# Kernel tuning notes

Measured on AMD Instinct MI355X. Metric: run time of the kernel, lower is better.

## Reference

```python
import jax, jax.numpy as jnp
import numpy as np

K = 3
KK = K * K


def conv3x3(x, w, b):
    # x: [B,C,H,W], w: [O,C,3,3]
    y = jax.lax.conv_general_dilated(x, w, (1, 1), ((1, 1), (1, 1)),
                                     dimension_numbers=('NCHW', 'OIHW', 'NCHW'))
    return y + b[None, :, None, None]


def deform_conv(x, offset, w, b):
    # torchvision.ops.deform_conv2d, 3x3, pad=1, stride=1, no mask.
    B, C, H, W = x.shape
    off = offset.reshape(B, KK, 2, H, W)  # per kernel tap: (dy, dx)
    ky = jnp.repeat(jnp.arange(K, dtype=x.dtype) - 1, K)  # [9]
    kx = jnp.tile(jnp.arange(K, dtype=x.dtype) - 1, K)
    py = jnp.arange(H, dtype=x.dtype)[None, None, :, None] + ky[None, :, None, None] + off[:, :, 0]
    px = jnp.arange(W, dtype=x.dtype)[None, None, None, :] + kx[None, :, None, None] + off[:, :, 1]
    y0 = jnp.floor(py)
    x0 = jnp.floor(px)
    wy = (py - y0)[:, None]  # [B,1,9,H,W]
    wx = (px - x0)[:, None]
    y0i = y0.astype(jnp.int32)
    x0i = x0.astype(jnp.int32)
    xf = x.reshape(B, C, H * W)

    def corner(yi, xi):
        valid = ((yi >= 0) & (yi < H) & (xi >= 0) & (xi < W))
        idx = jnp.clip(yi, 0, H - 1) * W + jnp.clip(xi, 0, W - 1)  # [B,9,H,W]
        g = jax.vmap(lambda xb, ib: xb[:, ib.reshape(-1)])(xf, idx)  # [B,C,9*H*W]
        return g.reshape(B, C, KK, H, W) * valid[:, None].astype(x.dtype)

    val = (corner(y0i, x0i) * (1 - wy) * (1 - wx)
           + corner(y0i, x0i + 1) * (1 - wy) * wx
           + corner(y0i + 1, x0i) * wy * (1 - wx)
           + corner(y0i + 1, x0i + 1) * wy * wx)  # [B,C,9,H,W]
    out = jnp.einsum('bckhw,ock->bohw', val, w.reshape(w.shape[0], C, KK))
    return out + b[None, :, None, None]


def se_gate(x, w1, b1, w2, b2):
    # global avg pool -> 1x1 conv -> relu -> 1x1 conv -> sigmoid -> scale
    m = x.mean((2, 3))  # [B,C]
    h = jax.nn.relu(jnp.einsum('bc,rc->br', m, w1) + b1)
    g = jax.nn.sigmoid(jnp.einsum('br,cr->bc', h, w2) + b2)
    return x * g[:, :, None, None]


def resize_bilinear(x, oh, ow):
    # F.interpolate(mode='bilinear', align_corners=False)
    B, C, H, W = x.shape

    def coords(n_in, n_out):
        src = (jnp.arange(n_out, dtype=x.dtype) + 0.5) * (n_in / n_out) - 0.5
        src = jnp.clip(src, 0.0, n_in - 1)
        i0 = jnp.floor(src).astype(jnp.int32)
        i1 = jnp.minimum(i0 + 1, n_in - 1)
        return i0, i1, (src - i0).astype(x.dtype)

    y0, y1, wy = coords(H, oh)
    x = x[:, :, y0, :] * (1 - wy)[None, None, :, None] + x[:, :, y1, :] * wy[None, None, :, None]
    c0, c1, wc = coords(W, ow)
    x = x[:, :, :, c0] * (1 - wc)[None, None, None, :] + x[:, :, :, c1] * wc[None, None, None, :]
    return x


def setup_inputs() -> dict:
    key = jax.random.key(0)
    ks = jax.random.split(key, 12)
    B, C, H, W = 4, 64, 128, 128
    L, O, R = 4, 64, 4  # levels, out_channels, reduction=64//16
    d = {
        'x': jax.random.normal(ks[0], (B, C, H, W), jnp.float32),
        'off_w': jax.random.normal(ks[1], (L, 2 * KK, C, 3, 3), jnp.float32) * 0.01,
        'off_b': jax.random.normal(ks[2], (L, 2 * KK), jnp.float32) * 0.01,
        'dc_w': jax.random.normal(ks[3], (L, O, C, 3, 3), jnp.float32) * 0.05,
        'dc_b': jax.random.normal(ks[4], (L, O), jnp.float32) * 0.05,
        'se_w1': jax.random.normal(ks[5], (L, R, O), jnp.float32) * 0.1,
        'se_b1': jax.random.normal(ks[6], (L, R), jnp.float32) * 0.1,
        'se_w2': jax.random.normal(ks[7], (L, O, R), jnp.float32) * 0.1,
        'se_b2': jax.random.normal(ks[8], (L, O), jnp.float32) * 0.1,
        'fuse_w': jax.random.normal(ks[9], (O, L * O), jnp.float32) * 0.05,
        'fuse_b': jax.random.normal(ks[10], (O,), jnp.float32) * 0.05,
    }
    return d


def reference(x, off_w, off_b, dc_w, dc_b, se_w1, se_b1, se_w2, se_b2, fuse_w, fuse_b):
    B, _, H, W = x.shape
    L = off_w.shape[0]
    cur = x
    feats = []
    for i in range(L):
        if i > 0:
            cur = resize_bilinear(cur, cur.shape[2] // 2, cur.shape[3] // 2)
        off = conv3x3(cur, off_w[i], off_b[i])
        cur = deform_conv(cur, off, dc_w[i], dc_b[i])
        cur = se_gate(cur, se_w1[i], se_b1[i], se_w2[i], se_b2[i])
        feats.append(resize_bilinear(cur, H, W))
    for i in range(L - 2, -1, -1):
        feats[i] = feats[i] + feats[i + 1]
    fused = jnp.concatenate(feats, axis=1)  # [B, L*O, H, W]
    return jnp.einsum('bchw,oc->bohw', fused, fuse_w) + fuse_b[None, :, None, None]
```

## Files before the change

### kernel.cpp

```cpp
#include <hip/hip_runtime.h>
#include <hip/hip_bf16.h>
#include <math.h>


constexpr int Bn = 4;

typedef __attribute__((ext_vector_type(8))) short short8;
typedef __attribute__((ext_vector_type(4))) float f32x4;
typedef __attribute__((ext_vector_type(4))) unsigned uint4v;
typedef __attribute__((ext_vector_type(4))) unsigned short ushort4v;

static __device__ __forceinline__ short f2b(float f){
  union { float f; unsigned u; } v; v.f = f;
  unsigned r = v.u + 0x7fffu + ((v.u >> 16) & 1u);
  return (short)(r >> 16);
}
static __device__ __forceinline__ unsigned f2b2(float x, float y){
  union { __hip_bfloat162 h; unsigned u; } cv;
  cv.h = __float22bfloat162_rn(make_float2(x, y));
  return cv.u;
}
static __device__ __forceinline__ float blo(unsigned u){ return __uint_as_float(u << 16); }
static __device__ __forceinline__ float bhi(unsigned u){ return __uint_as_float(u & 0xffff0000u); }

constexpr size_t OFF_CUR   = 0;
constexpr size_t OFF_DC    = OFF_CUR  + 4194304;
constexpr size_t OFF_T0    = OFF_DC   + 4194304;
constexpr size_t OFF_T1    = OFF_T0   + 4194304;
constexpr size_t OFF_T2    = OFF_T1   + 1048576;
constexpr size_t OFF_T3    = OFF_T2   + 262144;
constexpr size_t OFF_WSUMT = OFF_T3   + 65536;
constexpr size_t OFF_DCWT  = OFF_WSUMT + 8192;
constexpr size_t OFF_OWT   = OFF_DCWT  + 73728;
constexpr size_t OFF_SUMS  = OFF_OWT   + 36864;

__global__ __launch_bounds__(256) void prepcvt_k(
    const float* __restrict__ dc_w, const float* __restrict__ off_w,
    const float* __restrict__ fuse_w, float* __restrict__ ws,
    const float* __restrict__ x, unsigned* __restrict__ cur){
  __shared__ float t[64][65];
  {
    int i = blockIdx.x * 256 + threadIdx.x;
    short* dcwT  = (short*)(ws + OFF_DCWT);
    short* owT   = (short*)(ws + OFF_OWT);
    short* wsumT = (short*)(ws + OFF_WSUMT);
    if (i < 147456){
      int oc = i / 576, r = i % 576, k = r >> 6, c = r & 63;
      dcwT[i] = f2b(dc_w[(oc*64 + c)*9 + k]);
    } else if (i < 147456 + 73728){
      int tt = i - 147456;
      int lm = tt / 576, l = lm >> 5, m = lm & 31, r = tt % 576, k = r >> 6, c = r & 63;
      owT[tt] = (m < 18) ? f2b(off_w[((l*18 + m)*64 + c)*9 + k]) : (short)0;
    } else if (i < 147456 + 73728 + 16384){
      int tt = i - (147456 + 73728);
      int l = tt / 4096, r = tt % 4096, o = r / 64, c = r % 64;
      float s = 0.f;
      for (int jl = 0; jl <= l; jl++) s += fuse_w[o*256 + jl*64 + c];
      wsumT[tt] = f2b(s);
    } else if (i < 147456 + 73728 + 16384 + 65536){
      ws[OFF_SUMS + (i - (147456 + 73728 + 16384))] = 0.f;
    }
  }
  if (blockIdx.x < 1024){
    int tile = blockIdx.x;
    int b = tile >> 8, p0 = (tile & 255) << 6;
    int tx = threadIdx.x & 63, ty = threadIdx.x >> 6;
    #pragma unroll
    for (int c = ty; c < 64; c += 4)
      t[c][tx] = x[(((size_t)(b << 6) + c) << 14) + p0 + tx];
    __syncthreads();
    int u = threadIdx.x & 31, pr = threadIdx.x >> 5;
    #pragma unroll
    for (int i = 0; i < 8; i++){
      int pp = pr + i*8;
      unsigned v = f2b2(t[2*u][pp], t[2*u + 1][pp]);
      cur[((size_t)(b << 14) + p0 + pp)*32 + u] = v;
    }
  }
}

template<int H, int LVL>
__global__ __launch_bounds__(256, 3) void deform8_k(
    const unsigned* __restrict__ cur, const float* __restrict__ ws_all,
    const float* __restrict__ off_bias, const float* __restrict__ dc_bias,
    float* __restrict__ dc, float* __restrict__ sums){
  constexpr int W = H, P = H * W;
  constexpr int PITCHB = 584 * 2;
  constexpr int TPR8 = W/8, TPB8 = P/64;
  __shared__ __align__(16) short valA[16][584];
  __shared__ __align__(16) char  patchS[64*144];
  __shared__ __align__(16) float4 tapW[144];
  __shared__ __align__(8)  unsigned short tapIs[144][4];
  float* offsP = (float*)((char*)&valA[0][0] + 8192);
  const short* owt = (const short*)(ws_all + OFF_OWT) + LVL * 32 * 576;
  const short* dcw = (const short*)(ws_all + OFF_DCWT) + (size_t)LVL * 64 * 576;
  const int tid = threadIdx.x;
  const int wave = tid >> 6, lane = tid & 63;
  const int c0 = lane & 15, quad = lane >> 4, q4 = quad * 4;
  const int b = blockIdx.x / TPB8;
  const int rr = blockIdx.x % TPB8;
  const int hrow8 = (rr / TPR8) * 8, wcol8 = (rr % TPR8) * 8;
  const unsigned* curu = cur + (size_t)b * P * 32;
  const int n = wave*16 + c0;
  const float bt2 = dc_bias[LVL*64 + n];
  const int tk = tid % 9, tp = tid / 9;
  float oby = 0.f, obx = 0.f;
  if (tid < 144){
    oby = off_bias[LVL*18 + 2*tk];
    obx = off_bias[LVL*18 + 2*tk + 1];
  }
  const int pl = lane >> 3, cq = lane & 7;

  #pragma unroll 1
  for (int t = 0; t < 4; t++){
    const int srow = hrow8 + (t >> 1)*4, scol = wcol8 + (t & 1)*4;
    if (t) __syncthreads();

    #pragma unroll
    for (int i = 0; i < 2; i++){
      int pp = wave*16 + i*8 + pl;
      int R = pp >> 3, C = pp & 7;
      int yy = srow - 2 + R, xx = scol - 2 + C;
      bool v = ((unsigned)yy < (unsigned)H) & ((unsigned)xx < (unsigned)W);
      int idx = v ? (yy*W + xx) : 0;
      uint4 d = *(const uint4*)((const char*)curu + (size_t)idx*128 + cq*16);
      if (!v){ d.x = 0; d.y = 0; d.z = 0; d.w = 0; }
      *(uint4*)(patchS + pp*144 + cq*16) = d;
    }
    __syncthreads();

    {
      const int colw = wave & 1, kh = wave >> 1;
      const char* pb = patchS + (((c0 >> 2) + 1)*8 + (c0 & 3) + 1)*144 + quad*16;
      const short* wrow = owt + (colw*16 + c0)*576 + quad*8;
      f32x4 oacc = {0,0,0,0};
      if (kh == 0){
        #pragma unroll
        for (int kb = 0; kb < 9; kb++){
          const int tap = kb >> 1;
          short8 a  = *(const short8*)(pb + ((tap/3)*8 + (tap%3))*144 + (kb&1)*64);
          short8 bf = *(const short8*)&wrow[kb*32];
          oacc = __builtin_amdgcn_mfma_f32_16x16x32_bf16(a, bf, oacc, 0, 0, 0);
        }
      } else {
        #pragma unroll
        for (int kb = 0; kb < 9; kb++){
          const int kk = 9 + kb, tap = kk >> 1;
          short8 a  = *(const short8*)(pb + ((tap/3)*8 + (tap%3))*144 + (kk&1)*64);
          short8 bf = *(const short8*)&wrow[kk*32];
          oacc = __builtin_amdgcn_mfma_f32_16x16x32_bf16(a, bf, oacc, 0, 0, 0);
        }
      }
      int comp = colw*16 + c0;
      if (comp < 18){
        #pragma unroll
        for (int r = 0; r < 4; r++) offsP[kh*288 + (q4 + r)*18 + comp] = oacc[r];
      }
    }
    __syncthreads();

    if (tid < 144){
      int p = tp, k = tk;
      int h = srow + (p >> 2), w = scol + (p & 3);
      float oy = offsP[p*18 + 2*k]     + offsP[288 + p*18 + 2*k]     + oby;
      float ox = offsP[p*18 + 2*k + 1] + offsP[288 + p*18 + 2*k + 1] + obx;
      float py = (float)(h + k/3 - 1) + oy;
      float px = (float)(w + k%3 - 1) + ox;
      float y0f = floorf(py), x0f = floorf(px);
      float fy = py - y0f, fx = px - x0f;
      int y0 = (int)y0f, x0 = (int)x0f, y1 = y0 + 1, x1 = x0 + 1;
      bool vy0 = (y0 >= 0) & (y0 < H), vy1 = (y1 >= 0) & (y1 < H);
      bool vx0 = (x0 >= 0) & (x0 < W), vx1 = (x1 >= 0) & (x1 < W);
      int y0c = min(max(y0, 0), H-1), y1c = min(max(y1, 0), H-1);
      int x0c = min(max(x0, 0), W-1), x1c = min(max(x1, 0), W-1);
      float gy = 1.f - fy, gx = 1.f - fx;
      tapW[tid] = make_float4((vy0 & vx0) ? gy*gx : 0.f,
                              (vy0 & vx1) ? gy*fx : 0.f,
                              (vy1 & vx0) ? fy*gx : 0.f,
                              (vy1 & vx1) ? fy*fx : 0.f);
      int ry = y0 - srow + 2, rx = x0 - scol + 2;
      if (((unsigned)ry < 7u) & ((unsigned)rx < 7u)){
        tapIs[tid][0] = (unsigned short)(0x8000u | (ry*8 + rx));
      } else {
        tapIs[tid][0] = (unsigned short)(y0c*W + x0c);
        tapIs[tid][1] = (unsigned short)(y0c*W + x1c);
        tapIs[tid][2] = (unsigned short)(y1c*W + x0c);
        tapIs[tid][3] = (unsigned short)(y1c*W + x1c);
      }
    }
    __syncthreads();

    {
      const char* curc8 = (const char*)curu + c0*8;
      int T = wave*36 + quad;
      int p = wave*4, k = quad;
      #pragma unroll
      for (int i = 0; i < 9; i++){
        float4 wv = tapW[T];
        unsigned short t0 = tapIs[T][0];
        uint2 u0, u1, u2, u3;
        if (t0 & 0x8000u){
          const char* pb2 = patchS + (int)(t0 & 0x7fffu)*144 + c0*8;
          u0 = *(const uint2*)(pb2);
          u1 = *(const uint2*)(pb2 + 144);
          u2 = *(const uint2*)(pb2 + 144*8);
          u3 = *(const uint2*)(pb2 + 144*9);
        } else {
          uint2 tw = *(const uint2*)tapIs[T];
          u0 = *(const uint2*)(curc8 + ((size_t)(tw.x & 0xffffu) << 7));
          u1 = *(const uint2*)(curc8 + ((size_t)(tw.x >> 16)     << 7));
          u2 = *(const uint2*)(curc8 + ((size_t)(tw.y & 0xffffu) << 7));
          u3 = *(const uint2*)(curc8 + ((size_t)(tw.y >> 16)     << 7));
        }
        float a0 = wv.x*blo(u0.x) + wv.y*blo(u1.x) + wv.z*blo(u2.x) + wv.w*blo(u3.x);
        float a1 = wv.x*bhi(u0.x) + wv.y*bhi(u1.x) + wv.z*bhi(u2.x) + wv.w*bhi(u3.x);
        float a2 = wv.x*blo(u0.y) + wv.y*blo(u1.y) + wv.z*blo(u2.y) + wv.w*blo(u3.y);
        float a3 = wv.x*bhi(u0.y) + wv.y*bhi(u1.y) + wv.z*bhi(u2.y) + wv.w*bhi(u3.y);
        uint2 pk; pk.x = f2b2(a0, a1); pk.y = f2b2(a2, a3);
        *(uint2*)((char*)&valA[0][0] + p*PITCHB + k*128 + c0*8) = pk;
        T += 4; k += 4; if (k >= 9){ k -= 9; ++p; }
      }
    }
    __syncthreads();

    f32x4 d0 = {bt2, bt2, bt2, bt2}, d1 = {0,0,0,0};
    #pragma unroll
    for (int kb = 0; kb < 9; kb++){
      short8 a  = *(const short8*)&valA[c0][kb*32 + quad*8];
      short8 bf = *(const short8*)&dcw[n*576 + kb*32 + quad*8];
      d0 = __builtin_amdgcn_mfma_f32_16x16x32_bf16(a, bf, d0, 0, 0, 0);
    }
    #pragma unroll
    for (int kb = 9; kb < 18; kb++){
      short8 a  = *(const short8*)&valA[c0][kb*32 + quad*8];
      short8 bf = *(const short8*)&dcw[n*576 + kb*32 + quad*8];
      d1 = __builtin_amdgcn_mfma_f32_16x16x32_bf16(a, bf, d1, 0, 0, 0);
    }
    f32x4 acc;
    #pragma unroll
    for (int r = 0; r < 4; r++) acc[r] = d0[r] + d1[r];
    float* dcb = dc + ((size_t)b*P + (size_t)(srow + quad)*W + scol)*64;
    #pragma unroll
    for (int r = 0; r < 4; r++) dcb[r*64 + n] = acc[r];
    float s = acc[0] + acc[1] + acc[2] + acc[3];
    s += __shfl_xor(s, 16);
    s += __shfl_xor(s, 32);
    if (quad == 0) atomicAdd(&sums[(LVL*16 + (blockIdx.x & 15))*256 + (b << 6) + n], s);
  }
}

template<int H, int LVL>
__global__ __launch_bounds__(256, 7) void deform_k(
    const unsigned* __restrict__ cur, const float* __restrict__ ws_all,
    const float* __restrict__ off_bias, const float* __restrict__ dc_bias,
    float* __restrict__ dc, float* __restrict__ sums){
  constexpr int W = H, P = H * W;
  constexpr int PITCHB = 584 * 2;
  constexpr int TPR = W/4, TPB = P/16;
  __shared__ __align__(16) short valA[16][584];
  __shared__ __align__(16) float4 tapW[144];
  __shared__ __align__(8)  unsigned short tapIs[144][4];
  short* patch = &valA[0][0];
  float* offsP = (float*)((char*)&valA[0][0] + 8192);
  const short* owt = (const short*)(ws_all + OFF_OWT) + LVL * 32 * 576;
  const short* dcw = (const short*)(ws_all + OFF_DCWT) + (size_t)LVL * 64 * 576;
  const int tid = threadIdx.x;
  const int wave = tid >> 6, lane = tid & 63;
  const int c0 = lane & 15, quad = lane >> 4, q4 = quad * 4;
  const int b = blockIdx.x / TPB;
  const int rr = blockIdx.x % TPB;
  const int hrow = (rr / TPR) * 4, wcol = (rr % TPR) * 4;
  const unsigned* curu = cur + (size_t)b * P * 32;

  {
    #pragma unroll
    for (int i = 0; i < 3; i++){
      if (i < 2 || quad == 0){
        int p36 = wave*9 + i*4 + quad;
        int r6 = p36 / 6, c6 = p36 - r6*6;
        int yy = hrow - 1 + r6, xx = wcol - 1 + c6;
        bool v = ((unsigned)yy < (unsigned)H) & ((unsigned)xx < (unsigned)W);
        int idx = v ? (yy*W + xx) : 0;
        uint2 d = *(const uint2*)(curu + (size_t)idx*32 + c0*2);
        if (!v){ d.x = 0u; d.y = 0u; }
        *(uint2*)(patch + p36*72 + c0*4) = d;
      }
    }
  }
  __syncthreads();

  {
    const int colw = wave & 1, kh = wave >> 1;
    const char* pb = (const char*)patch + ((c0 >> 2) * 6 + (c0 & 3)) * 144 + quad * 16;
    const short* wrow = owt + (colw*16 + c0)*576 + quad*8;
    f32x4 oacc = {0,0,0,0};
    if (kh == 0){
      #pragma unroll
      for (int kb = 0; kb < 9; kb++){
        const int tap = kb >> 1;
        short8 a  = *(const short8*)(pb + ((tap/3)*864 + (tap%3)*144 + (kb&1)*64));
        short8 bf = *(const short8*)&wrow[kb*32];
        oacc = __builtin_amdgcn_mfma_f32_16x16x32_bf16(a, bf, oacc, 0, 0, 0);
      }
    } else {
      #pragma unroll
      for (int kb = 0; kb < 9; kb++){
        const int kk = 9 + kb, tap = kk >> 1;
        short8 a  = *(const short8*)(pb + ((tap/3)*864 + (tap%3)*144 + (kk&1)*64));
        short8 bf = *(const short8*)&wrow[kk*32];
        oacc = __builtin_amdgcn_mfma_f32_16x16x32_bf16(a, bf, oacc, 0, 0, 0);
      }
    }
    int comp = colw*16 + c0;
    if (comp < 18){
      #pragma unroll
      for (int r = 0; r < 4; r++) offsP[kh*288 + (q4 + r)*18 + comp] = oacc[r];
    }
  }
  __syncthreads();

  if (tid < 144){
    int p = tid / 9, k = tid % 9;
    int h = hrow + (p >> 2), w = wcol + (p & 3);
    float oy = offsP[p*18 + 2*k]     + offsP[288 + p*18 + 2*k]     + off_bias[LVL*18 + 2*k];
    float ox = offsP[p*18 + 2*k + 1] + offsP[288 + p*18 + 2*k + 1] + off_bias[LVL*18 + 2*k + 1];
    float py = (float)(h + k/3 - 1) + oy;
    float px = (float)(w + k%3 - 1) + ox;
    float y0f = floorf(py), x0f = floorf(px);
    float fy = py - y0f, fx = px - x0f;
    int y0 = (int)y0f, x0 = (int)x0f, y1 = y0 + 1, x1 = x0 + 1;
    bool vy0 = (y0 >= 0) & (y0 < H), vy1 = (y1 >= 0) & (y1 < H);
    bool vx0 = (x0 >= 0) & (x0 < W), vx1 = (x1 >= 0) & (x1 < W);
    int y0c = min(max(y0, 0), H-1), y1c = min(max(y1, 0), H-1);
    int x0c = min(max(x0, 0), W-1), x1c = min(max(x1, 0), W-1);
    float gy = 1.f - fy, gx = 1.f - fx;
    tapW[tid] = make_float4((vy0 & vx0) ? gy*gx : 0.f,
                            (vy0 & vx1) ? gy*fx : 0.f,
                            (vy1 & vx0) ? fy*gx : 0.f,
                            (vy1 & vx1) ? fy*fx : 0.f);
    ushort4v ti = { (unsigned short)(y0c*W + x0c), (unsigned short)(y0c*W + x1c),
                    (unsigned short)(y1c*W + x0c), (unsigned short)(y1c*W + x1c) };
    *(ushort4v*)tapIs[tid] = ti;
  }
  __syncthreads();

  {
    const char* curc8 = (const char*)curu + c0*8;
    int T = wave*36 + quad;
    int p = T/9, k = T - p*9;
    #pragma unroll
    for (int i = 0; i < 9; i++){
      float4 wv = tapW[T];
      uint2 tw = *(const uint2*)tapIs[T];
      uint2 u0 = *(const uint2*)(curc8 + ((size_t)(tw.x & 0xffffu) << 7));
      uint2 u1 = *(const uint2*)(curc8 + ((size_t)(tw.x >> 16) << 7));
      uint2 u2 = *(const uint2*)(curc8 + ((size_t)(tw.y & 0xffffu) << 7));
      uint2 u3 = *(const uint2*)(curc8 + ((size_t)(tw.y >> 16) << 7));
      float a0 = wv.x*blo(u0.x) + wv.y*blo(u1.x) + wv.z*blo(u2.x) + wv.w*blo(u3.x);
      float a1 = wv.x*bhi(u0.x) + wv.y*bhi(u1.x) + wv.z*bhi(u2.x) + wv.w*bhi(u3.x);
      float a2 = wv.x*blo(u0.y) + wv.y*blo(u1.y) + wv.z*blo(u2.y) + wv.w*blo(u3.y);
      float a3 = wv.x*bhi(u0.y) + wv.y*bhi(u1.y) + wv.z*bhi(u2.y) + wv.w*bhi(u3.y);
      uint2 pk; pk.x = f2b2(a0, a1); pk.y = f2b2(a2, a3);
      *(uint2*)((char*)&valA[0][0] + p*PITCHB + k*128 + c0*8) = pk;
      T += 4; k += 4; if (k >= 9){ k -= 9; ++p; }
    }
  }
  __syncthreads();

  const int n = wave*16 + c0;
  float bt2 = dc_bias[LVL*64 + n];
  f32x4 d0 = {bt2, bt2, bt2, bt2}, d1 = {0,0,0,0};
  #pragma unroll
  for (int kb = 0; kb < 9; kb++){
    short8 a  = *(const short8*)&valA[c0][kb*32 + quad*8];
    short8 bf = *(const short8*)&dcw[n*576 + kb*32 + quad*8];
    d0 = __builtin_amdgcn_mfma_f32_16x16x32_bf16(a, bf, d0, 0, 0, 0);
  }
  #pragma unroll
  for (int kb = 9; kb < 18; kb++){
    short8 a  = *(const short8*)&valA[c0][kb*32 + quad*8];
    short8 bf = *(const short8*)&dcw[n*576 + kb*32 + quad*8];
    d1 = __builtin_amdgcn_mfma_f32_16x16x32_bf16(a, bf, d1, 0, 0, 0);
  }
  f32x4 acc;
  #pragma unroll
  for (int r = 0; r < 4; r++) acc[r] = d0[r] + d1[r];
  float* dcb = dc + ((size_t)b*P + (size_t)(hrow + quad)*W + wcol)*64;
  #pragma unroll
  for (int r = 0; r < 4; r++) dcb[r*64 + n] = acc[r];
  float s = acc[0] + acc[1] + acc[2] + acc[3];
  s += __shfl_xor(s, 16);
  s += __shfl_xor(s, 32);
  if (quad == 0) atomicAdd(&sums[(LVL*16 + (blockIdx.x & 15))*256 + (b << 6) + n], s);
}

template<int W, int LVL>
__global__ __launch_bounds__(256) void fuse_gd_k(
    const float* __restrict__ dcv, const float* __restrict__ sums,
    const float* __restrict__ se_w1, const float* __restrict__ se_b1,
    const float* __restrict__ se_w2, const float* __restrict__ se_b2,
    const float* __restrict__ ws_all, float* __restrict__ tmp, unsigned* __restrict__ curn){
  constexpr int P = W * W;
  constexpr bool POOL = (LVL < 3);
  constexpr float invP = 1.f / (float)P;
  __shared__ __align__(16) float fS[64][68];
  __shared__ __align__(16) float gsh[64];
  const short* wsl = (const short*)(ws_all + OFF_WSUMT) + LVL * 4096;
  const int tid = threadIdx.x, wave = tid >> 6, lane = tid & 63;
  const int c0 = lane & 15, quad = lane >> 4, q4 = quad * 4;
  int b, rp = 0, cs = 0;
  if (POOL){
    constexpr int tilesPerB = P / 64, tilesPerRow = W / 32;
    b = blockIdx.x / tilesPerB;
    int r = blockIdx.x % tilesPerB;
    rp = r / tilesPerRow; cs = r % tilesPerRow;
  } else {
    b = (blockIdx.x * 64) / P;
  }

  {
    int sg = tid >> 6, c = tid & 63;
    float part = 0.f;
    #pragma unroll
    for (int s = 0; s < 4; s++) part += sums[(LVL*16 + sg*4 + s)*256 + (b << 6) + c];
    fS[sg][c] = part;
    __syncthreads();
    if (tid < 64){
      int r = tid & 3, j = tid >> 2;
      float hp = 0.f;
      #pragma unroll
      for (int q = 0; q < 4; q++){
        int cq = j*4 + q;
        float m = (fS[0][cq] + fS[1][cq] + fS[2][cq] + fS[3][cq]) * invP;
        hp += m * se_w1[(LVL*4 + r)*64 + cq];
      }
      hp += __shfl_xor(hp, 4);  hp += __shfl_xor(hp, 8);
      hp += __shfl_xor(hp, 16); hp += __shfl_xor(hp, 32);
      float hr = fmaxf(hp + se_b1[LVL*4 + r], 0.f);
      float a = se_b2[LVL*64 + tid];
      #pragma unroll
      for (int r2 = 0; r2 < 4; r2++)
        a += __shfl(hr, r2) * se_w2[(LVL*64 + tid)*4 + r2];
      gsh[tid] = 1.f / (1.f + expf(-a));
    }
    __syncthreads();
  }

  float4 g4 = *(const float4*)&gsh[c0*4];
  #pragma unroll
  for (int i = 0; i < 4; i++){
    int lp = wave*16 + (lane >> 4) + i*4;
    size_t gpix = POOL ? ((size_t)b*P + (size_t)(2*rp + (lp >> 5))*W + cs*32 + (lp & 31))
                       : ((size_t)blockIdx.x*64 + lp);
    float4 d = *(const float4*)&dcv[gpix*64 + c0*4];
    float4 v = make_float4(d.x*g4.x, d.y*g4.y, d.z*g4.z, d.w*g4.w);
    *(float4*)&fS[lp][c0*4] = v;
  }
  __syncthreads();
  f32x4 acc[4] = {{0,0,0,0},{0,0,0,0},{0,0,0,0},{0,0,0,0}};
  #pragma unroll
  for (int kb = 0; kb < 2; kb++){
    float4 lo = *(const float4*)&fS[wave*16 + c0][kb*32 + quad*8];
    float4 hi = *(const float4*)&fS[wave*16 + c0][kb*32 + quad*8 + 4];
    uint4v ua = {f2b2(lo.x, lo.y), f2b2(lo.z, lo.w), f2b2(hi.x, hi.y), f2b2(hi.z, hi.w)};
    short8 a = __builtin_bit_cast(short8, ua);
    #pragma unroll
    for (int t = 0; t < 4; t++){
      short8 bf = *(const short8*)&wsl[(t*16 + c0)*64 + kb*32 + quad*8];
      acc[t] = __builtin_amdgcn_mfma_f32_16x16x32_bf16(a, bf, acc[t], 0, 0, 0);
    }
  }
  #pragma unroll
  for (int t = 0; t < 4; t++){
    int n = t*16 + c0;
    size_t plane = ((size_t)(b << 6) + n) * P;
    size_t pix = POOL ? ((size_t)(2*rp + (wave >> 1))*W + cs*32 + (wave & 1)*16 + q4)
                      : ((size_t)(blockIdx.x*64) - (size_t)b*P + wave*16 + q4);
    *(f32x4*)&tmp[plane + pix] = acc[t];
  }
  if constexpr (POOL){
    int j = tid >> 4, uu = tid & 15;
    float4 p0 = *(const float4*)&fS[2*j][uu*4];
    float4 p1 = *(const float4*)&fS[2*j + 1][uu*4];
    float4 p2 = *(const float4*)&fS[32 + 2*j][uu*4];
    float4 p3 = *(const float4*)&fS[33 + 2*j][uu*4];
    float4 av = make_float4(0.25f*(p0.x + p1.x + p2.x + p3.x),
                            0.25f*(p0.y + p1.y + p2.y + p3.y),
                            0.25f*(p0.z + p1.z + p2.z + p3.z),
                            0.25f*(p0.w + p1.w + p2.w + p3.w));
    uint2 pv = make_uint2(f2b2(av.x, av.y), f2b2(av.z, av.w));
    *(uint2*)&curn[((size_t)b*(P/4) + (size_t)rp*(W/2) + cs*16 + j)*32 + uu*2] = pv;
  }
}

__global__ void final_k(const float* __restrict__ ws_all, const float* __restrict__ fuse_bias,
                        float* __restrict__ out){
  int i = blockIdx.x * 256 + threadIdx.x;
  int w = i & 127, h = (i >> 7) & 127, o = (i >> 14) & 63, b = i >> 20;
  float acc = fuse_bias[o] + ws_all[OFF_T0 + (((size_t)(b << 6) + o) << 14) + (h << 7) + w];
  const float* tarr[3] = {ws_all + OFF_T1, ws_all + OFF_T2, ws_all + OFF_T3};
  #pragma unroll
  for (int li = 0; li < 3; li++){
    int l = li + 1, Hl = 128 >> l;
    float scale = 1.0f / (float)(1 << l);
    float sy = fminf(fmaxf((h + 0.5f)*scale - 0.5f, 0.f), (float)(Hl - 1));
    float sx = fminf(fmaxf((w + 0.5f)*scale - 0.5f, 0.f), (float)(Hl - 1));
    int y0 = (int)sy, x0 = (int)sx;
    float fy = sy - y0, fx = sx - x0;
    int y1 = min(y0 + 1, Hl - 1), x1 = min(x0 + 1, Hl - 1);
    const float* tb = tarr[li] + (size_t)((b << 6) + o) * Hl * Hl;
    float v00 = tb[y0*Hl + x0], v01 = tb[y0*Hl + x1];
    float v10 = tb[y1*Hl + x0], v11 = tb[y1*Hl + x1];
    acc += (1.f-fy)*((1.f-fx)*v00 + fx*v01) + fy*((1.f-fx)*v10 + fx*v11);
  }
  out[i] = acc;
}

extern "C" void kernel_launch(void* const* d_in, const int* in_sizes, int n_in,
                              void* d_out, int out_size, void* d_ws, size_t ws_size,
                              hipStream_t stream){
  (void)in_sizes; (void)n_in; (void)out_size; (void)ws_size;
  const float* x      = (const float*)d_in[0];
  const float* off_w  = (const float*)d_in[1];
  const float* off_b  = (const float*)d_in[2];
  const float* dc_w   = (const float*)d_in[3];
  const float* dc_b   = (const float*)d_in[4];
  const float* se_w1  = (const float*)d_in[5];
  const float* se_b1  = (const float*)d_in[6];
  const float* se_w2  = (const float*)d_in[7];
  const float* se_b2  = (const float*)d_in[8];
  const float* fuse_w = (const float*)d_in[9];
  const float* fuse_b = (const float*)d_in[10];
  float* out = (float*)d_out;
  float* ws = (float*)d_ws;
  unsigned* cur = (unsigned*)(ws + OFF_CUR);
  float* dc   = ws + OFF_DC;
  float* tmp[4] = {ws + OFF_T0, ws + OFF_T1, ws + OFF_T2, ws + OFF_T3};
  float* sums = ws + OFF_SUMS;

  prepcvt_k<<<(303104 + 255)/256, 256, 0, stream>>>(dc_w, off_w, fuse_w, ws, x, cur);

  deform8_k<128,0><<<1024, 256, 0, stream>>>(cur, ws, off_b, dc_b, dc, sums);
  fuse_gd_k<128,0><<<1024, 256, 0, stream>>>(dc, sums, se_w1, se_b1, se_w2, se_b2, ws, tmp[0], cur);
  deform_k<64,1><<<1024, 256, 0, stream>>>(cur, ws, off_b, dc_b, dc, sums);
  fuse_gd_k<64,1><<<256, 256, 0, stream>>>(dc, sums, se_w1, se_b1, se_w2, se_b2, ws, tmp[1], cur);
  deform_k<32,2><<<256, 256, 0, stream>>>(cur, ws, off_b, dc_b, dc, sums);
  fuse_gd_k<32,2><<<64, 256, 0, stream>>>(dc, sums, se_w1, se_b1, se_w2, se_b2, ws, tmp[2], cur);
  deform_k<16,3><<<64, 256, 0, stream>>>(cur, ws, off_b, dc_b, dc, sums);
  fuse_gd_k<16,3><<<16, 256, 0, stream>>>(dc, sums, se_w1, se_b1, se_w2, se_b2, ws, tmp[3], nullptr);

  final_k<<<16384, 256, 0, stream>>>(ws, fuse_b, out);
}
```

Before: 219.5 us.

## Split level-0 deformable conv into offset kernel and gather-GEMM kernel

The fused level-0 deform8 kernel becomes two kernels. offs_k computes the offset convolution for 4x4 tiles and writes the sampling coordinates to a global workspace buffer. dgemm_k reads those coordinates, gathers the bilinear samples straight from global memory and runs the 3x3 GEMM with MFMA. The aim is to shrink per-block LDS and register use so more blocks fit per CU (launch bounds 8 and 7 instead of 3). The cost is an extra kernel launch, a round trip of the offset buffer through global memory, and all gathers going to global/L2 instead of partly coming from the LDS patch.

```diff
diff --git a/kernel.cpp b/kernel.cpp
--- a/kernel.cpp
+++ b/kernel.cpp
@@ -24,6 +24,7 @@
 static __device__ __forceinline__ float bhi(unsigned u){ return __uint_as_float(u & 0xffff0000u); }
 
 constexpr size_t OFF_CUR   = 0;
+constexpr size_t OFF_OFFS  = OFF_CUR  + 2097152;
 constexpr size_t OFF_DC    = OFF_CUR  + 4194304;
 constexpr size_t OFF_T0    = OFF_DC   + 4194304;
 constexpr size_t OFF_T1    = OFF_T0   + 4194304;
@@ -80,92 +81,109 @@
 }
 
 template<int H, int LVL>
-__global__ __launch_bounds__(256, 3) void deform8_k(
+__global__ __launch_bounds__(256, 8) void offs_k(
+    const unsigned* __restrict__ cur, float* __restrict__ ws,
+    const float* __restrict__ off_bias){
+  constexpr int W = H, P = H * W;
+  constexpr int TPR = W/4, TPB = P/16;
+  __shared__ __align__(16) short patch[36*72];
+  __shared__ float offsP[2*16*18];
+  const short* owt = (const short*)(ws + OFF_OWT) + LVL * 32 * 576;
+  float2* offsOut = (float2*)(ws + OFF_OFFS);
+  const int tid = threadIdx.x;
+  const int wave = tid >> 6, lane = tid & 63;
+  const int c0 = lane & 15, quad = lane >> 4, q4 = quad * 4;
+  const int b = blockIdx.x / TPB;
+  const int rr = blockIdx.x % TPB;
+  const int hrow = (rr / TPR) * 4, wcol = (rr % TPR) * 4;
+  const unsigned* curu = cur + (size_t)b * P * 32;
+
+  {
+    #pragma unroll
+    for (int i = 0; i < 3; i++){
+      if (i < 2 || quad == 0){
+        int p36 = wave*9 + i*4 + quad;
+        int r6 = p36 / 6, c6 = p36 - r6*6;
+        int yy = hrow - 1 + r6, xx = wcol - 1 + c6;
+        bool v = ((unsigned)yy < (unsigned)H) & ((unsigned)xx < (unsigned)W);
+        int idx = v ? (yy*W + xx) : 0;
+        uint2 d = *(const uint2*)(curu + (size_t)idx*32 + c0*2);
+        if (!v){ d.x = 0u; d.y = 0u; }
+        *(uint2*)(patch + p36*72 + c0*4) = d;
+      }
+    }
+  }
+  __syncthreads();
+
+  {
+    const int colw = wave & 1, kh = wave >> 1;
+    const char* pb = (const char*)patch + ((c0 >> 2) * 6 + (c0 & 3)) * 144 + quad * 16;
+    const short* wrow = owt + (colw*16 + c0)*576 + quad*8;
+    f32x4 oacc = {0,0,0,0};
+    if (kh == 0){
+      #pragma unroll
+      for (int kb = 0; kb < 9; kb++){
+        const int tap = kb >> 1;
+        short8 a  = *(const short8*)(pb + ((tap/3)*864 + (tap%3)*144 + (kb&1)*64));
+        short8 bf = *(const short8*)&wrow[kb*32];
+        oacc = __builtin_amdgcn_mfma_f32_16x16x32_bf16(a, bf, oacc, 0, 0, 0);
+      }
+    } else {
+      #pragma unroll
+      for (int kb = 0; kb < 9; kb++){
+        const int kk = 9 + kb, tap = kk >> 1;
+        short8 a  = *(const short8*)(pb + ((tap/3)*864 + (tap%3)*144 + (kk&1)*64));
+        short8 bf = *(const short8*)&wrow[kk*32];
+        oacc = __builtin_amdgcn_mfma_f32_16x16x32_bf16(a, bf, oacc, 0, 0, 0);
+      }
+    }
+    int comp = colw*16 + c0;
+    if (comp < 18){
+      #pragma unroll
+      for (int r = 0; r < 4; r++) offsP[kh*288 + (q4 + r)*18 + comp] = oacc[r];
+    }
+  }
+  __syncthreads();
+
+  if (tid < 144){
+    int p = tid / 9, k = tid % 9;
+    int h = hrow + (p >> 2), w = wcol + (p & 3);
+    float oy = offsP[p*18 + 2*k]     + offsP[288 + p*18 + 2*k]     + off_bias[LVL*18 + 2*k];
+    float ox = offsP[p*18 + 2*k + 1] + offsP[288 + p*18 + 2*k + 1] + off_bias[LVL*18 + 2*k + 1];
+    float py = (float)(h + k/3 - 1) + oy;
+    float px = (float)(w + k%3 - 1) + ox;
+    offsOut[(size_t)(b*P + h*W + w)*9 + k] = make_float2(py, px);
+  }
+}
+
+template<int H, int LVL>
+__global__ __launch_bounds__(256, 7) void dgemm_k(
     const unsigned* __restrict__ cur, const float* __restrict__ ws_all,
-    const float* __restrict__ off_bias, const float* __restrict__ dc_bias,
+    const float* __restrict__ dc_bias,
     float* __restrict__ dc, float* __restrict__ sums){
   constexpr int W = H, P = H * W;
   constexpr int PITCHB = 584 * 2;
-  constexpr int TPR8 = W/8, TPB8 = P/64;
+  constexpr int TPR = W/4, TPB = P/16;
   __shared__ __align__(16) short valA[16][584];
-  __shared__ __align__(16) char  patchS[64*144];
-  __shared__ __align__(16) float4 tapW[144];
-  __shared__ __align__(8)  unsigned short tapIs[144][4];
-  float* offsP = (float*)((char*)&valA[0][0] + 8192);
-  const short* owt = (const short*)(ws_all + OFF_OWT) + LVL * 32 * 576;
   const short* dcw = (const short*)(ws_all + OFF_DCWT) + (size_t)LVL * 64 * 576;
+  const float2* offs = (const float2*)(ws_all + OFF_OFFS);
   const int tid = threadIdx.x;
   const int wave = tid >> 6, lane = tid & 63;
-  const int c0 = lane & 15, quad = lane >> 4, q4 = quad * 4;
-  const int b = blockIdx.x / TPB8;
-  const int rr = blockIdx.x % TPB8;
-  const int hrow8 = (rr / TPR8) * 8, wcol8 = (rr % TPR8) * 8;
+  const int c0 = lane & 15, quad = lane >> 4;
+  const int b = blockIdx.x / TPB;
+  const int rr = blockIdx.x % TPB;
+  const int hrow = (rr / TPR) * 4, wcol = (rr % TPR) * 4;
   const unsigned* curu = cur + (size_t)b * P * 32;
-  const int n = wave*16 + c0;
-  const float bt2 = dc_bias[LVL*64 + n];
-  const int tk = tid % 9, tp = tid / 9;
-  float oby = 0.f, obx = 0.f;
-  if (tid < 144){
-    oby = off_bias[LVL*18 + 2*tk];
-    obx = off_bias[LVL*18 + 2*tk + 1];
-  }
-  const int pl = lane >> 3, cq = lane & 7;
-
-  #pragma unroll 1
-  for (int t = 0; t < 4; t++){
-    const int srow = hrow8 + (t >> 1)*4, scol = wcol8 + (t & 1)*4;
-    if (t) __syncthreads();
-
-    #pragma unroll
-    for (int i = 0; i < 2; i++){
-      int pp = wave*16 + i*8 + pl;
-      int R = pp >> 3, C = pp & 7;
-      int yy = srow - 2 + R, xx = scol - 2 + C;
-      bool v = ((unsigned)yy < (unsigned)H) & ((unsigned)xx < (unsigned)W);
-      int idx = v ? (yy*W + xx) : 0;
-      uint4 d = *(const uint4*)((const char*)curu + (size_t)idx*128 + cq*16);
-      if (!v){ d.x = 0; d.y = 0; d.z = 0; d.w = 0; }
-      *(uint4*)(patchS + pp*144 + cq*16) = d;
-    }
-    __syncthreads();
-
-    {
-      const int colw = wave & 1, kh = wave >> 1;
-      const char* pb = patchS + (((c0 >> 2) + 1)*8 + (c0 & 3) + 1)*144 + quad*16;
-      const short* wrow = owt + (colw*16 + c0)*576 + quad*8;
-      f32x4 oacc = {0,0,0,0};
-      if (kh == 0){
-        #pragma unroll
-        for (int kb = 0; kb < 9; kb++){
-          const int tap = kb >> 1;
-          short8 a  = *(const short8*)(pb + ((tap/3)*8 + (tap%3))*144 + (kb&1)*64);
-          short8 bf = *(const short8*)&wrow[kb*32];
-          oacc = __builtin_amdgcn_mfma_f32_16x16x32_bf16(a, bf, oacc, 0, 0, 0);
-        }
-      } else {
-        #pragma unroll
-        for (int kb = 0; kb < 9; kb++){
-          const int kk = 9 + kb, tap = kk >> 1;
-          short8 a  = *(const short8*)(pb + ((tap/3)*8 + (tap%3))*144 + (kk&1)*64);
-          short8 bf = *(const short8*)&wrow[kk*32];
-          oacc = __builtin_amdgcn_mfma_f32_16x16x32_bf16(a, bf, oacc, 0, 0, 0);
-        }
-      }
-      int comp = colw*16 + c0;
-      if (comp < 18){
-        #pragma unroll
-        for (int r = 0; r < 4; r++) offsP[kh*288 + (q4 + r)*18 + comp] = oacc[r];
-      }
-    }
-    __syncthreads();
-
-    if (tid < 144){
-      int p = tp, k = tk;
-      int h = srow + (p >> 2), w = scol + (p & 3);
-      float oy = offsP[p*18 + 2*k]     + offsP[288 + p*18 + 2*k]     + oby;
-      float ox = offsP[p*18 + 2*k + 1] + offsP[288 + p*18 + 2*k + 1] + obx;
-      float py = (float)(h + k/3 - 1) + oy;
-      float px = (float)(w + k%3 - 1) + ox;
+  const char* curc8 = (const char*)curu + c0*8;
+
+  {
+    int T = wave*36 + quad;
+    int p = T/9, k = T - p*9;
+    #pragma unroll
+    for (int i = 0; i < 9; i++){
+      int h = hrow + (p >> 2), w = wcol + (p & 3);
+      float2 pc = offs[(size_t)(b*P + h*W + w)*9 + k];
+      float py = pc.x, px = pc.y;
       float y0f = floorf(py), x0f = floorf(px);
       float fy = py - y0f, fx = px - x0f;
       int y0 = (int)y0f, x0 = (int)x0f, y1 = y0 + 1, x1 = x0 + 1;
@@ -174,79 +192,52 @@
       int y0c = min(max(y0, 0), H-1), y1c = min(max(y1, 0), H-1);
       int x0c = min(max(x0, 0), W-1), x1c = min(max(x1, 0), W-1);
       float gy = 1.f - fy, gx = 1.f - fx;
-      tapW[tid] = make_float4((vy0 & vx0) ? gy*gx : 0.f,
-                              (vy0 & vx1) ? gy*fx : 0.f,
-                              (vy1 & vx0) ? fy*gx : 0.f,
-                              (vy1 & vx1) ? fy*fx : 0.f);
-      int ry = y0 - srow + 2, rx = x0 - scol + 2;
-      if (((unsigned)ry < 7u) & ((unsigned)rx < 7u)){
-        tapIs[tid][0] = (unsigned short)(0x8000u | (ry*8 + rx));
-      } else {
-        tapIs[tid][0] = (unsigned short)(y0c*W + x0c);
-        tapIs[tid][1] = (unsigned short)(y0c*W + x1c);
-        tapIs[tid][2] = (unsigned short)(y1c*W + x0c);
-        tapIs[tid][3] = (unsigned short)(y1c*W + x1c);
-      }
-    }
-    __syncthreads();
-
-    {
-      const char* curc8 = (const char*)curu + c0*8;
-      int T = wave*36 + quad;
-      int p = wave*4, k = quad;
-      #pragma unroll
-      for (int i = 0; i < 9; i++){
-        float4 wv = tapW[T];
-        unsigned short t0 = tapIs[T][0];
-        uint2 u0, u1, u2, u3;
-        if (t0 & 0x8000u){
-          const char* pb2 = patchS + (int)(t0 & 0x7fffu)*144 + c0*8;
-          u0 = *(const uint2*)(pb2);
-          u1 = *(const uint2*)(pb2 + 144);
-          u2 = *(const uint2*)(pb2 + 144*8);
-          u3 = *(const uint2*)(pb2 + 144*9);
-        } else {
-          uint2 tw = *(const uint2*)tapIs[T];
-          u0 = *(const uint2*)(curc8 + ((size_t)(tw.x & 0xffffu) << 7));
-          u1 = *(const uint2*)(curc8 + ((size_t)(tw.x >> 16)     << 7));
-          u2 = *(const uint2*)(curc8 + ((size_t)(tw.y & 0xffffu) << 7));
-          u3 = *(const uint2*)(curc8 + ((size_t)(tw.y >> 16)     << 7));
-        }
-        float a0 = wv.x*blo(u0.x) + wv.y*blo(u1.x) + wv.z*blo(u2.x) + wv.w*blo(u3.x);
-        float a1 = wv.x*bhi(u0.x) + wv.y*bhi(u1.x) + wv.z*bhi(u2.x) + wv.w*bhi(u3.x);
-        float a2 = wv.x*blo(u0.y) + wv.y*blo(u1.y) + wv.z*blo(u2.y) + wv.w*blo(u3.y);
-        float a3 = wv.x*bhi(u0.y) + wv.y*bhi(u1.y) + wv.z*bhi(u2.y) + wv.w*bhi(u3.y);
-        uint2 pk; pk.x = f2b2(a0, a1); pk.y = f2b2(a2, a3);
-        *(uint2*)((char*)&valA[0][0] + p*PITCHB + k*128 + c0*8) = pk;
-        T += 4; k += 4; if (k >= 9){ k -= 9; ++p; }
-      }
-    }
-    __syncthreads();
-
-    f32x4 d0 = {bt2, bt2, bt2, bt2}, d1 = {0,0,0,0};
-    #pragma unroll
-    for (int kb = 0; kb < 9; kb++){
-      short8 a  = *(const short8*)&valA[c0][kb*32 + quad*8];
-      short8 bf = *(const short8*)&dcw[n*576 + kb*32 + quad*8];
-      d0 = __builtin_amdgcn_mfma_f32_16x16x32_bf16(a, bf, d0, 0, 0, 0);
-    }
-    #pragma unroll
-    for (int kb = 9; kb < 18; kb++){
-      short8 a  = *(const short8*)&valA[c0][kb*32 + quad*8];
-      short8 bf = *(const short8*)&dcw[n*576 + kb*32 + quad*8];
-      d1 = __builtin_amdgcn_mfma_f32_16x16x32_bf16(a, bf, d1, 0, 0, 0);
-    }
-    f32x4 acc;
-    #pragma unroll
-    for (int r = 0; r < 4; r++) acc[r] = d0[r] + d1[r];
-    float* dcb = dc + ((size_t)b*P + (size_t)(srow + quad)*W + scol)*64;
-    #pragma unroll
-    for (int r = 0; r < 4; r++) dcb[r*64 + n] = acc[r];
-    float s = acc[0] + acc[1] + acc[2] + acc[3];
-    s += __shfl_xor(s, 16);
-    s += __shfl_xor(s, 32);
-    if (quad == 0) atomicAdd(&sums[(LVL*16 + (blockIdx.x & 15))*256 + (b << 6) + n], s);
-  }
+      float w00 = (vy0 & vx0) ? gy*gx : 0.f;
+      float w01 = (vy0 & vx1) ? gy*fx : 0.f;
+      float w10 = (vy1 & vx0) ? fy*gx : 0.f;
+      float w11 = (vy1 & vx1) ? fy*fx : 0.f;
+      uint2 u0 = *(const uint2*)(curc8 + ((size_t)(y0c*W + x0c) << 7));
+      uint2 u1 = *(const uint2*)(curc8 + ((size_t)(y0c*W + x1c) << 7));
+      uint2 u2 = *(const uint2*)(curc8 + ((size_t)(y1c*W + x0c) << 7));
+      uint2 u3 = *(const uint2*)(curc8 + ((size_t)(y1c*W + x1c) << 7));
+      float a0 = w00*blo(u0.x) + w01*blo(u1.x) + w10*blo(u2.x) + w11*blo(u3.x);
+      float a1 = w00*bhi(u0.x) + w01*bhi(u1.x) + w10*bhi(u2.x) + w11*bhi(u3.x);
+      float a2 = w00*blo(u0.y) + w01*blo(u1.y) + w10*blo(u2.y) + w11*blo(u3.y);
+      float a3 = w00*bhi(u0.y) + w01*bhi(u1.y) + w10*bhi(u2.y) + w11*bhi(u3.y);
+      uint2 pk; pk.x = f2b2(a0, a1); pk.y = f2b2(a2, a3);
+      *(uint2*)((char*)&valA[0][0] + p*PITCHB + k*128 + c0*8) = pk;
+      k += 4; if (k >= 9){ k -= 9; ++p; }
+    }
+  }
+  __syncthreads();
+
+  const int n = wave*16 + c0;
+  const int q4 = quad * 4;
+  float bt2 = dc_bias[LVL*64 + n];
+  f32x4 d0 = {bt2, bt2, bt2, bt2}, d1 = {0,0,0,0};
+  #pragma unroll
+  for (int kb = 0; kb < 9; kb++){
+    short8 a  = *(const short8*)&valA[c0][kb*32 + quad*8];
+    short8 bf = *(const short8*)&dcw[n*576 + kb*32 + quad*8];
+    d0 = __builtin_amdgcn_mfma_f32_16x16x32_bf16(a, bf, d0, 0, 0, 0);
+  }
+  #pragma unroll
+  for (int kb = 9; kb < 18; kb++){
+    short8 a  = *(const short8*)&valA[c0][kb*32 + quad*8];
+    short8 bf = *(const short8*)&dcw[n*576 + kb*32 + quad*8];
+    d1 = __builtin_amdgcn_mfma_f32_16x16x32_bf16(a, bf, d1, 0, 0, 0);
+  }
+  f32x4 acc;
+  #pragma unroll
+  for (int r = 0; r < 4; r++) acc[r] = d0[r] + d1[r];
+  float* dcb = dc + ((size_t)b*P + (size_t)(hrow + quad)*W + wcol)*64;
+  #pragma unroll
+  for (int r = 0; r < 4; r++) dcb[r*64 + n] = acc[r];
+  float s = acc[0] + acc[1] + acc[2] + acc[3];
+  s += __shfl_xor(s, 16);
+  s += __shfl_xor(s, 32);
+  if (quad == 0) atomicAdd(&sums[(LVL*16 + (blockIdx.x & 15))*256 + (b << 6) + n], s);
+  (void)q4;
 }
 
 template<int H, int LVL>
@@ -540,7 +531,8 @@
 
   prepcvt_k<<<(303104 + 255)/256, 256, 0, stream>>>(dc_w, off_w, fuse_w, ws, x, cur);
 
-  deform8_k<128,0><<<1024, 256, 0, stream>>>(cur, ws, off_b, dc_b, dc, sums);
+  offs_k<128,0><<<4096, 256, 0, stream>>>(cur, ws, off_b);
+  dgemm_k<128,0><<<4096, 256, 0, stream>>>(cur, ws, dc_b, dc, sums);
   fuse_gd_k<128,0><<<1024, 256, 0, stream>>>(dc, sums, se_w1, se_b1, se_w2, se_b2, ws, tmp[0], cur);
   deform_k<64,1><<<1024, 256, 0, stream>>>(cur, ws, off_b, dc_b, dc, sums);
   fuse_gd_k<64,1><<<256, 256, 0, stream>>>(dc, sums, se_w1, se_b1, se_w2, se_b2, ws, tmp[1], cur);
```

Measured after the change: 244.1 us. 1.11x slower.
